# Optimization experiments

Hardware: AMD Instinct MI355X
Metric: run time of the kernel (lower is better)

Reference implementation:

```python
import jax, jax.numpy as jnp
import numpy as np
import math

DEPTH = 12
LAMBDA_INIT = 0.8 - 0.6 * math.exp(-0.3 * DEPTH)
EPS = 1e-5


def setup_inputs() -> dict:
    key = jax.random.key(0)
    ks = jax.random.split(key, 10)
    B, S, E, H, D = 2, 2048, 1024, 8, 64
    query = jax.random.normal(ks[0], (B, S, E), dtype=jnp.float32)
    init = 0.02
    Wq = jax.random.normal(ks[1], (E, 2 * H * D), dtype=jnp.float32) * init
    Wk = jax.random.normal(ks[2], (E, 2 * H * D), dtype=jnp.float32) * init
    Wv = jax.random.normal(ks[3], (E, 2 * H * D), dtype=jnp.float32) * init
    Wo = jax.random.normal(ks[4], (2 * H * D, E), dtype=jnp.float32) * init
    lq1 = jax.random.normal(ks[5], (D,), dtype=jnp.float32) * 0.1
    lk1 = jax.random.normal(ks[6], (D,), dtype=jnp.float32) * 0.1
    lq2 = jax.random.normal(ks[7], (D,), dtype=jnp.float32) * 0.1
    lk2 = jax.random.normal(ks[8], (D,), dtype=jnp.float32) * 0.1
    subln_w = jnp.ones((2 * D,), dtype=jnp.float32)
    return {"query": query, "Wq": Wq, "Wk": Wk, "Wv": Wv, "Wo": Wo,
            "lq1": lq1, "lk1": lk1, "lq2": lq2, "lk2": lk2, "subln_w": subln_w}


def reference(query, Wq, Wk, Wv, Wo, lq1, lk1, lq2, lk2, subln_w):
    B, S, E = query.shape
    D = lq1.shape[0]
    H = Wq.shape[1] // (2 * D)
    scaling = D ** -0.5
    # projections -> (B, 2H, S, D) for q/k, (B, H, S, 2D) for v
    q = (query @ Wq).reshape(B, S, 2 * H, D).transpose(0, 2, 1, 3) * scaling
    k = (query @ Wk).reshape(B, S, 2 * H, D).transpose(0, 2, 1, 3)
    v = (query @ Wv).reshape(B, S, H, 2 * D).transpose(0, 2, 1, 3)
    score = jnp.einsum('bhqd,bhkd->bhqk', q, k)  # (B, 2H, S, S)
    score = jnp.nan_to_num(score)
    score = jax.nn.softmax(score.astype(jnp.float32), axis=-1).astype(score.dtype)
    lambda_1 = jnp.exp(jnp.sum(lq1 * lk1))
    lambda_2 = jnp.exp(jnp.sum(lq2 * lk2))
    lambda_full = lambda_1 - lambda_2 + LAMBDA_INIT
    score = score.reshape(B, H, 2, S, S)
    score = score[:, :, 0] - lambda_full * score[:, :, 1]  # (B, H, S, S)
    attn = jnp.einsum('bhqk,bhkd->bhqd', score, v)  # (B, H, S, 2D)
    # RMSNorm over last dim (computed in fp32, cast back), affine weight
    af = attn.astype(jnp.float32)
    attn = (af * jax.lax.rsqrt(jnp.mean(af * af, axis=-1, keepdims=True) + EPS)).astype(attn.dtype)
    attn = attn * subln_w
    attn = attn * (1.0 - LAMBDA_INIT)
    attn = attn.transpose(0, 2, 1, 3).reshape(B, S, H * 2 * D)
    return attn @ Wo
```

## Files before the change

### kernel.cpp

```cpp
#include <hip/hip_runtime.h>

typedef __attribute__((ext_vector_type(4))) float f32x4;
typedef __attribute__((ext_vector_type(8))) short bf16x8;
typedef unsigned short u16;
typedef unsigned int u32;

#define LAMBDA_INIT 0.7836057665311429f
#define ONE_MINUS_LI 0.2163942334688571f
#define QSCALE_LOG2 0.1803368801111137f

__device__ __forceinline__ u16 f2b(float f){
  union { float f; unsigned u; } v; v.f = f;
  unsigned r = v.u + 0x7fff + ((v.u >> 16) & 1);
  return (u16)(r >> 16);
}

__device__ __forceinline__ f32x4 mfma16(bf16x8 a, bf16x8 b, f32x4 c){
  return __builtin_amdgcn_mfma_f32_16x16x32_bf16(a, b, c, 0, 0, 0);
}

__device__ __forceinline__ float exp2_raw(float x){
  float r;
  asm("v_exp_f32 %0, %1" : "=v"(r) : "v"(x));
  return r;
}

__device__ __forceinline__ void async16(void* lds, const void* g){
  __builtin_amdgcn_global_load_lds((const __attribute__((address_space(1))) void*)g,
                                   (__attribute__((address_space(3))) void*)lds, 16, 0, 0);
}

__global__ void prep(const float* __restrict__ query,
                     const float* __restrict__ Wq, const float* __restrict__ Wk,
                     const float* __restrict__ Wv, const float* __restrict__ Wo,
                     u16* __restrict__ Xbf, u16* __restrict__ Wqkvt, u16* __restrict__ Wot){
  int z = blockIdx.z;
  int c0 = blockIdx.x * 32, r0 = blockIdx.y * 32;
  int tx = threadIdx.x, ty = threadIdx.y;
  if (z == 4){
    #pragma unroll
    for (int k = 0; k < 4; k++){
      size_t base = (size_t)(k * 1024 + r0) * 1024;
      for (int i = 0; i < 32; i += 8)
        Xbf[base + (size_t)(ty + i) * 1024 + c0 + tx] =
            f2b(query[base + (size_t)(ty + i) * 1024 + c0 + tx]);
    }
    return;
  }
  __shared__ float t[32][33];
  const float* in = (z == 0) ? Wq : (z == 1) ? Wk : (z == 2) ? Wv : Wo;
  u16* out = (z < 3) ? (Wqkvt + (size_t)z * 1048576) : Wot;
  for (int i = 0; i < 32; i += 8) t[ty + i][tx] = in[(size_t)(r0 + ty + i) * 1024 + c0 + tx];
  __syncthreads();
  for (int i = 0; i < 32; i += 8) out[(size_t)(c0 + ty + i) * 1024 + r0 + tx] = f2b(t[tx][ty + i]);
}

template<int PERM>
__global__ void transpose_bf16(const u16* __restrict__ in, u16* __restrict__ out, int R, int C){
  __shared__ u16 t[32][34];
  int c0 = blockIdx.x * 32, r0 = blockIdx.y * 32;
  size_t boff = (size_t)blockIdx.z * R * C;
  int tx = threadIdx.x, ty = threadIdx.y;
  for (int i = 0; i < 32; i += 8) t[ty + i][tx] = in[boff + (size_t)(r0 + ty + i) * C + c0 + tx];
  __syncthreads();
  for (int i = 0; i < 32; i += 8){
    int dv = c0 + ty + i, s = r0 + tx;
    int sx;
    if (PERM){
      int sl = s & 63;
      int n = sl >> 4, g = (sl >> 2) & 3, r = sl & 3;
      int pos = (s & ~63) | ((n >> 1) << 5) | (g << 3) | ((n & 1) << 2) | r;
      sx = (pos & ~63) | ((((pos >> 3) & 7) ^ (dv & 7)) << 3) | (pos & 7);
    } else sx = s;
    out[boff + (size_t)dv * R + sx] = t[tx][ty + i];
  }
}

template<int BN, int EPI>
__global__ __launch_bounds__(256, 2) void gemm_async(
    const u16* __restrict__ A, const u16* __restrict__ Bt, float* __restrict__ Cp,
    u16* __restrict__ Qo, u16* __restrict__ Ko, u16* __restrict__ Vo,
    int M, int N, int K, int gm){
  constexpr int BCH = BN / 32;
  __shared__ u16 As[2][128 * 64];
  __shared__ u16 Bs[2][BN * 64];
  int tid = threadIdx.x, w = tid >> 6, lane = tid & 63;
  int l16 = lane & 15, grp = lane >> 4;
  int wr = w >> 1, wc = w & 1;
  int nwg = gridDim.x, bid = blockIdx.x;
  int idx = (bid & 7) * (nwg >> 3) + (bid >> 3);
  int m0 = (idx & (gm - 1)) * 128, n0 = (idx / gm) * BN;

  int sr = lane >> 3;
  int sc = ((lane & 7) ^ sr) << 3;
  const u16* pA = A  + (size_t)(m0 + w * 8 + sr) * K + sc;
  const u16* pB = Bt + (size_t)(n0 + w * 8 + sr) * K + sc;

  f32x4 acc[4][BN / 32] = {};

#define STAGEG(bb, k0) do{                                             \
    _Pragma("unroll")                                                  \
    for (int i = 0; i < 4; i++)                                        \
      async16(&As[bb][i * 2048 + w * 512], pA + (k0) + (size_t)i * 32 * K); \
    _Pragma("unroll")                                                  \
    for (int i = 0; i < BCH; i++)                                      \
      async16(&Bs[bb][i * 2048 + w * 512], pB + (k0) + (size_t)i * 32 * K); \
  } while(0)

  STAGEG(0, 0);
  int niter = K >> 6;
  for (int kt = 0; kt < niter; kt++){
    int cur = kt & 1;
    if (kt < niter - 1){
      STAGEG(cur ^ 1, (kt + 1) << 6);
      if constexpr (BN == 128) asm volatile("s_waitcnt vmcnt(8)" ::: "memory");
      else                     asm volatile("s_waitcnt vmcnt(6)" ::: "memory");
    } else {
      asm volatile("s_waitcnt vmcnt(0)" ::: "memory");
    }
    __builtin_amdgcn_s_barrier();

    const u16* Ap = As[cur];
    const u16* Bp = Bs[cur];
    #pragma unroll
    for (int kk = 0; kk < 2; kk++){
      bf16x8 a[4], b[BN / 32];
      #pragma unroll
      for (int m = 0; m < 4; m++){
        int r = wr * 64 + m * 16 + l16;
        a[m] = *(const bf16x8*)&Ap[r * 64 + (((kk * 4 + grp) ^ (r & 7)) << 3)];
      }
      #pragma unroll
      for (int n = 0; n < BCH; n++){
        int r = wc * (BN / 2) + n * 16 + l16;
        b[n] = *(const bf16x8*)&Bp[r * 64 + (((kk * 4 + grp) ^ (r & 7)) << 3)];
      }
      #pragma unroll
      for (int m = 0; m < 4; m++)
        #pragma unroll
        for (int n = 0; n < BCH; n++)
          acc[m][n] = mfma16(a[m], b[n], acc[m][n]);
    }
    if (kt < niter - 1){
      asm volatile("s_waitcnt lgkmcnt(0)" ::: "memory");
      __builtin_amdgcn_s_barrier();
    }
  }
#undef STAGEG

  if constexpr (EPI == 0){
    #pragma unroll
    for (int m = 0; m < 4; m++)
      #pragma unroll
      for (int n = 0; n < BCH; n++)
        #pragma unroll
        for (int r = 0; r < 4; r++)
          Cp[(size_t)(m0 + wr * 64 + m * 16 + grp * 4 + r) * N + n0 + wc * (BN / 2) + n * 16 + l16]
            = acc[m][n][r];
  } else {
    int proj = n0 >> 10;
    #pragma unroll
    for (int m = 0; m < 4; m++){
      int row = m0 + wr * 64 + m * 16 + grp * 4;
      #pragma unroll
      for (int n = 0; n < BCH; n++){
        int col = n0 + wc * (BN / 2) + n * 16 + l16;
        int cn = col & 1023;
        if (proj == 0){
          #pragma unroll
          for (int r = 0; r < 4; r++)
            Qo[(size_t)(row + r) * 1024 + cn] = f2b(acc[m][n][r] * QSCALE_LOG2);
        } else if (proj == 1){
          #pragma unroll
          for (int r = 0; r < 4; r++){
            int cs = (cn & ~63) | ((((cn >> 3) & 7) ^ ((row + r) & 7)) << 3) | (cn & 7);
            Ko[(size_t)(row + r) * 1024 + cs] = f2b(acc[m][n][r]);
          }
        } else {
          #pragma unroll
          for (int r = 0; r < 4; r++)
            Vo[(size_t)(row + r) * 1024 + cn] = f2b(acc[m][n][r]);
        }
      }
    }
  }
}

__global__ __launch_bounds__(256, 2) void diff_attn(
    const u16* __restrict__ Qb, const u16* __restrict__ Kb, const u16* __restrict__ Vt,
    const float* __restrict__ lq1, const float* __restrict__ lk1,
    const float* __restrict__ lq2, const float* __restrict__ lk2,
    const float* __restrict__ slw, u16* __restrict__ attnb){
  __shared__ u16 Ksh[2][2][64 * 64];
  __shared__ u16 Vsh[2][128 * 64];
  __shared__ float lam_s;

  int tid = threadIdx.x, w = tid >> 6, lane = tid & 63;
  int l16 = lane & 15, grp = lane >> 4;
  int bid = blockIdx.x;
  int h = bid & 7, qt = (bid >> 3) & 31, b = bid >> 8;
  int tb = b * 2048 + qt * 64;

  if (tid < 64){
    float p1 = lq1[tid] * lk1[tid], p2 = lq2[tid] * lk2[tid];
    #pragma unroll
    for (int m = 32; m >= 1; m >>= 1){ p1 += __shfl_xor(p1, m); p2 += __shfl_xor(p2, m); }
    if (tid == 0) lam_s = __expf(p1) - __expf(p2) + LAMBDA_INIT;
  }

  const u16* gK1 = Kb + (size_t)(b * 2048 + w * 16 + (lane >> 3)) * 1024 + 128 * h + (lane & 7) * 8;
  const u16* gK2 = gK1 + 64;
  const u16* gV  = Vt + (size_t)(b * 1024 + 128 * h + w * 32 + (lane >> 3)) * 2048 + (lane & 7) * 8;

  bf16x8 q1[2], q2[2];
  {
    const u16* qr = Qb + (size_t)(tb + w * 16 + l16) * 1024 + 128 * h;
    q1[0] = *(const bf16x8*)(qr + grp * 8);
    q1[1] = *(const bf16x8*)(qr + 32 + grp * 8);
    q2[0] = *(const bf16x8*)(qr + 64 + grp * 8);
    q2[1] = *(const bf16x8*)(qr + 96 + grp * 8);
  }

  bf16x8 ones;
  #pragma unroll
  for (int i = 0; i < 8; i++) ones[i] = (short)0x3F80;

#define STAGE_K(bb, PK1, PK2) do{                           \
    async16(&Ksh[bb][0][w * 1024],       (PK1));            \
    async16(&Ksh[bb][0][w * 1024 + 512], (PK1) + 8192);     \
    async16(&Ksh[bb][1][w * 1024],       (PK2));            \
    async16(&Ksh[bb][1][w * 1024 + 512], (PK2) + 8192);     \
  } while(0)
#define STAGE_V(bb, PV) do{                                 \
    async16(&Vsh[bb][w * 2048],          (PV));             \
    async16(&Vsh[bb][w * 2048 + 512],    (PV) + 16384);     \
    async16(&Vsh[bb][w * 2048 + 1024],   (PV) + 32768);     \
    async16(&Vsh[bb][w * 2048 + 1536],   (PV) + 49152);     \
  } while(0)

  int xo0 = ((grp ^ (l16 & 7)) << 3);
  int xo1 = (((4 + grp) ^ (l16 & 7)) << 3);

#define QKCOMP(bb, S1, S2) do{                                           \
    const u16* K1p = Ksh[bb][0];                                         \
    const u16* K2p = Ksh[bb][1];                                         \
    _Pragma("unroll")                                                    \
    for (int n = 0; n < 4; n++){ S1[n] = (f32x4){0,0,0,0}; S2[n] = (f32x4){0,0,0,0}; } \
    _Pragma("unroll")                                                    \
    for (int n = 0; n < 4; n++){                                         \
      int rb = (n * 16 + l16) << 6;                                      \
      bf16x8 k1a = *(const bf16x8*)&K1p[rb + xo0];                       \
      bf16x8 k1b = *(const bf16x8*)&K1p[rb + xo1];                       \
      bf16x8 k2a = *(const bf16x8*)&K2p[rb + xo0];                       \
      bf16x8 k2b = *(const bf16x8*)&K2p[rb + xo1];                       \
      S1[n] = mfma16(k1a, q1[0], S1[n]);                                 \
      S1[n] = mfma16(k1b, q1[1], S1[n]);                                 \
      S2[n] = mfma16(k2a, q2[0], S2[n]);                                 \
      S2[n] = mfma16(k2b, q2[1], S2[n]);                                 \
    }                                                                    \
  } while(0)

#define EXPPACK(S, PB) do{                                               \
    float p[16];                                                         \
    _Pragma("unroll")                                                    \
    for (int n = 0; n < 4; n++)                                          \
      _Pragma("unroll")                                                  \
      for (int r = 0; r < 4; r++) p[n * 4 + r] = exp2_raw(S[n][r] - 4.0f); \
    union { u32 wd[4]; bf16x8 v; } u0, u1;                               \
    _Pragma("unroll")                                                    \
    for (int j = 0; j < 4; j++){                                         \
      asm("v_cvt_pk_bf16_f32 %0, %1, %2" : "=v"(u0.wd[j]) : "v"(p[2 * j]),     "v"(p[2 * j + 1])); \
      asm("v_cvt_pk_bf16_f32 %0, %1, %2" : "=v"(u1.wd[j]) : "v"(p[8 + 2 * j]), "v"(p[9 + 2 * j])); \
    }                                                                    \
    PB[0] = u0.v; PB[1] = u1.v;                                          \
  } while(0)

  STAGE_K(0, gK1, gK2); STAGE_V(0, gV);
  gK1 += 65536; gK2 += 65536; gV += 64;
  STAGE_K(1, gK1, gK2); STAGE_V(1, gV);
  gK1 += 65536; gK2 += 65536; gV += 64;
  __syncthreads();

  f32x4 s1c[4], s2c[4], s1n[4], s2n[4];
  QKCOMP(0, s1c, s2c);

  f32x4 O1[9] = {}, O2[9] = {};

  for (int kt = 0; kt < 32; kt++){
    int cur = kt & 1;
    if (kt < 30){
      STAGE_K(cur, gK1, gK2);
      gK1 += 65536; gK2 += 65536;
      asm volatile("s_waitcnt vmcnt(4)" ::: "memory");
    } else {
      asm volatile("s_waitcnt vmcnt(0)" ::: "memory");
    }
    __builtin_amdgcn_s_barrier();

    if (kt < 31) QKCOMP(cur ^ 1, s1n, s2n);
    bf16x8 pbA[2], pbB[2];
    EXPPACK(s1c, pbA);
    EXPPACK(s2c, pbB);

    const u16* Vp = Vsh[cur];
    __builtin_amdgcn_s_setprio(1);
    #pragma unroll
    for (int kk = 0; kk < 2; kk++){
      int xo = kk ? xo1 : xo0;
      #pragma unroll
      for (int n = 0; n < 8; n++){
        bf16x8 av = *(const bf16x8*)&Vp[((n * 16 + l16) << 6) + xo];
        O1[n] = mfma16(av, pbA[kk], O1[n]);
        O2[n] = mfma16(av, pbB[kk], O2[n]);
      }
      O1[8] = mfma16(ones, pbA[kk], O1[8]);
      O2[8] = mfma16(ones, pbB[kk], O2[8]);
    }
    __builtin_amdgcn_s_setprio(0);

    if (kt < 31){
      asm volatile("s_waitcnt lgkmcnt(0)" ::: "memory");
      __builtin_amdgcn_s_barrier();
      if (kt < 30){
        STAGE_V(cur, gV);
        gV += 64;
      }
      #pragma unroll
      for (int n = 0; n < 4; n++){ s1c[n] = s1n[n]; s2c[n] = s2n[n]; }
    }
  }
#undef STAGE_K
#undef STAGE_V
#undef QKCOMP
#undef EXPPACK

  float lam = lam_s;
  float i1 = 1.f / O1[8][0], i2 = lam / O2[8][0];
  float x[8][4], ss = 0.f;
  #pragma unroll
  for (int n = 0; n < 8; n++)
    #pragma unroll
    for (int r = 0; r < 4; r++){
      float v = O1[n][r] * i1 - O2[n][r] * i2;
      x[n][r] = v; ss += v * v;
    }
  ss += __shfl_xor(ss, 16);
  ss += __shfl_xor(ss, 32);
  float ri = rsqrtf(ss * (1.f / 128.f) + 1e-5f);
  int row = tb + w * 16 + l16;
  #pragma unroll
  for (int n = 0; n < 8; n++){
    float4 sw = *(const float4*)&slw[n * 16 + grp * 4];
    ushort4 o;
    o.x = f2b(x[n][0] * ri * sw.x * ONE_MINUS_LI);
    o.y = f2b(x[n][1] * ri * sw.y * ONE_MINUS_LI);
    o.z = f2b(x[n][2] * ri * sw.z * ONE_MINUS_LI);
    o.w = f2b(x[n][3] * ri * sw.w * ONE_MINUS_LI);
    *(ushort4*)&attnb[(size_t)row * 1024 + h * 128 + n * 16 + grp * 4] = o;
  }
}

extern "C" void kernel_launch(void* const* d_in, const int* in_sizes, int n_in,
                              void* d_out, int out_size, void* d_ws, size_t ws_size,
                              hipStream_t stream){
  const float* query = (const float*)d_in[0];
  const float* Wq = (const float*)d_in[1];
  const float* Wk = (const float*)d_in[2];
  const float* Wv = (const float*)d_in[3];
  const float* Wo = (const float*)d_in[4];
  const float* lq1 = (const float*)d_in[5];
  const float* lk1 = (const float*)d_in[6];
  const float* lq2 = (const float*)d_in[7];
  const float* lk2 = (const float*)d_in[8];
  const float* slw = (const float*)d_in[9];

  char* ws = (char*)d_ws;
  u16* Xbf   = (u16*)(ws + 0);
  u16* Wqkvt = (u16*)(ws + 8388608);
  u16* Wot   = (u16*)(ws + 14680064);
  u16* Qbuf  = (u16*)(ws + 16777216);
  u16* Kbuf  = (u16*)(ws + 25165824);
  u16* Vbuf  = (u16*)(ws + 33554432);
  u16* Vtr   = (u16*)(ws + 41943040);
  u16* Attn  = (u16*)(ws + 50331648);

  prep<<<dim3(32, 32, 5), dim3(32, 8), 0, stream>>>(query, Wq, Wk, Wv, Wo,
                                                    Xbf, Wqkvt, Wot);

  gemm_async<128, 1><<<768, 256, 0, stream>>>(Xbf, Wqkvt, nullptr, Qbuf, Kbuf, Vbuf,
                                              4096, 3072, 1024, 32);

  transpose_bf16<1><<<dim3(32, 64, 2), dim3(32, 8), 0, stream>>>(Vbuf, Vtr, 2048, 1024);

  diff_attn<<<512, 256, 0, stream>>>(Qbuf, Kbuf, Vtr, lq1, lk1, lq2, lk2, slw, Attn);

  gemm_async<64, 0><<<512, 256, 0, stream>>>(Attn, Wot, (float*)d_out,
                                             nullptr, nullptr, nullptr,
                                             4096, 1024, 1024, 32);
}
```

Before: 131.3 us.

## Triple-buffer V tiles and issue V loads alongside K loads

```diff
diff --git a/kernel.cpp b/kernel.cpp
--- a/kernel.cpp
+++ b/kernel.cpp
@@ -192,8 +192,7 @@
     const float* __restrict__ lq2, const float* __restrict__ lk2,
     const float* __restrict__ slw, u16* __restrict__ attnb){
   __shared__ u16 Ksh[2][2][64 * 64];
-  __shared__ u16 Vsh[2][128 * 64];
-  __shared__ float lam_s;
+  __shared__ u16 Vsh[3][128 * 64];
 
   int tid = threadIdx.x, w = tid >> 6, lane = tid & 63;
   int l16 = lane & 15, grp = lane >> 4;
@@ -201,11 +200,12 @@
   int h = bid & 7, qt = (bid >> 3) & 31, b = bid >> 8;
   int tb = b * 2048 + qt * 64;
 
-  if (tid < 64){
-    float p1 = lq1[tid] * lk1[tid], p2 = lq2[tid] * lk2[tid];
+  float lam;
+  {
+    float p1 = lq1[lane] * lk1[lane], p2 = lq2[lane] * lk2[lane];
     #pragma unroll
     for (int m = 32; m >= 1; m >>= 1){ p1 += __shfl_xor(p1, m); p2 += __shfl_xor(p2, m); }
-    if (tid == 0) lam_s = __expf(p1) - __expf(p2) + LAMBDA_INIT;
+    lam = __expf(p1) - __expf(p2) + LAMBDA_INIT;
   }
 
   const u16* gK1 = Kb + (size_t)(b * 2048 + w * 16 + (lane >> 3)) * 1024 + 128 * h + (lane & 7) * 8;
@@ -231,11 +231,11 @@
     async16(&Ksh[bb][1][w * 1024],       (PK2));            \
     async16(&Ksh[bb][1][w * 1024 + 512], (PK2) + 8192);     \
   } while(0)
-#define STAGE_V(bb, PV) do{                                 \
-    async16(&Vsh[bb][w * 2048],          (PV));             \
-    async16(&Vsh[bb][w * 2048 + 512],    (PV) + 16384);     \
-    async16(&Vsh[bb][w * 2048 + 1024],   (PV) + 32768);     \
-    async16(&Vsh[bb][w * 2048 + 1536],   (PV) + 49152);     \
+#define STAGE_V(ss, PV) do{                                 \
+    async16(&Vsh[ss][w * 2048],          (PV));             \
+    async16(&Vsh[ss][w * 2048 + 512],    (PV) + 16384);     \
+    async16(&Vsh[ss][w * 2048 + 1024],   (PV) + 32768);     \
+    async16(&Vsh[ss][w * 2048 + 1536],   (PV) + 49152);     \
   } while(0)
 
   int xo0 = ((grp ^ (l16 & 7)) << 3);
@@ -283,26 +283,31 @@
 
   f32x4 s1c[4], s2c[4], s1n[4], s2n[4];
   QKCOMP(0, s1c, s2c);
+  __syncthreads();
 
   f32x4 O1[9] = {}, O2[9] = {};
+  int vc = 0, vnx = 2;
 
   for (int kt = 0; kt < 32; kt++){
-    int cur = kt & 1;
+    int kc = kt & 1;
     if (kt < 30){
-      STAGE_K(cur, gK1, gK2);
-      gK1 += 65536; gK2 += 65536;
+      STAGE_K(kc, gK1, gK2);
+      STAGE_V(vnx, gV);
+      gK1 += 65536; gK2 += 65536; gV += 64;
+      asm volatile("s_waitcnt vmcnt(8)" ::: "memory");
+    } else if (kt == 30){
       asm volatile("s_waitcnt vmcnt(4)" ::: "memory");
     } else {
       asm volatile("s_waitcnt vmcnt(0)" ::: "memory");
     }
     __builtin_amdgcn_s_barrier();
 
-    if (kt < 31) QKCOMP(cur ^ 1, s1n, s2n);
+    if (kt < 31) QKCOMP(kc ^ 1, s1n, s2n);
     bf16x8 pbA[2], pbB[2];
     EXPPACK(s1c, pbA);
     EXPPACK(s2c, pbB);
 
-    const u16* Vp = Vsh[cur];
+    const u16* Vp = Vsh[vc];
     __builtin_amdgcn_s_setprio(1);
     #pragma unroll
     for (int kk = 0; kk < 2; kk++){
@@ -321,20 +326,17 @@
     if (kt < 31){
       asm volatile("s_waitcnt lgkmcnt(0)" ::: "memory");
       __builtin_amdgcn_s_barrier();
-      if (kt < 30){
-        STAGE_V(cur, gV);
-        gV += 64;
-      }
       #pragma unroll
       for (int n = 0; n < 4; n++){ s1c[n] = s1n[n]; s2c[n] = s2n[n]; }
     }
+    vc = (vc == 2) ? 0 : vc + 1;
+    vnx = (vnx == 2) ? 0 : vnx + 1;
   }
 #undef STAGE_K
 #undef STAGE_V
 #undef QKCOMP
 #undef EXPPACK
 
-  float lam = lam_s;
   float i1 = 1.f / O1[8][0], i2 = lam / O2[8][0];
   float x[8][4], ss = 0.f;
   #pragma unroll
```

New measurement: 132.5 us. No clear change (+0.9%).
